# Kernel tuning notes

Measured on AMD Instinct MI355X. Metric: run time of the kernel, lower is better.

## Reference

```python
import jax, jax.numpy as jnp
import numpy as np

N_NODES = 50000
N_EDGES = 500000
IN_CH = 256
HID = 64
HEADS = 8
OUT_CH = 16
NEG_SLOPE = 0.2  # PyG GATConv default


def setup_inputs() -> dict:
    key = jax.random.key(0)
    ks = jax.random.split(key, 10)
    x = jax.random.normal(ks[0], (N_NODES, IN_CH), dtype=jnp.float32)
    edge_index = jax.random.randint(ks[1], (2, N_EDGES), 0, N_NODES, dtype=jnp.int64)
    s1 = 1.0 / np.sqrt(IN_CH)
    W1 = jax.random.uniform(ks[2], (IN_CH, HEADS * HID), jnp.float32, -s1, s1)
    att_src1 = jax.random.normal(ks[3], (HEADS, HID), dtype=jnp.float32) * 0.1
    att_dst1 = jax.random.normal(ks[4], (HEADS, HID), dtype=jnp.float32) * 0.1
    b1 = jnp.zeros((HEADS * HID,), jnp.float32)
    s2 = 1.0 / np.sqrt(HEADS * HID)
    W2 = jax.random.uniform(ks[5], (HEADS * HID, OUT_CH), jnp.float32, -s2, s2)
    att_src2 = jax.random.normal(ks[6], (1, OUT_CH), dtype=jnp.float32) * 0.1
    att_dst2 = jax.random.normal(ks[7], (1, OUT_CH), dtype=jnp.float32) * 0.1
    b2 = jnp.zeros((OUT_CH,), jnp.float32)
    return {"x": x, "edge_index": edge_index, "W1": W1, "att_src1": att_src1,
            "att_dst1": att_dst1, "b1": b1, "W2": W2, "att_src2": att_src2,
            "att_dst2": att_dst2, "b2": b2}


def _gat_conv(x, src, dst, W, att_src, att_dst, bias, heads, out_ch, concat, n_nodes):
    # Linear transform: [N, H, C]
    h = (x @ W).reshape(n_nodes, heads, out_ch)
    # Per-node attention logits: [N, H]
    a_src = jnp.einsum('nhc,hc->nh', h, att_src)
    a_dst = jnp.einsum('nhc,hc->nh', h, att_dst)
    # Edge-wise attention score (message src -> dst): [E, H]
    e = jax.nn.leaky_relu(a_src[src] + a_dst[dst], NEG_SLOPE)
    # Segment softmax over incoming edges of each destination node
    emax = jax.ops.segment_max(e, dst, num_segments=n_nodes)  # [N, H]
    emax = jnp.where(jnp.isfinite(emax), emax, 0.0)
    e = jnp.exp(e - emax[dst])
    denom = jax.ops.segment_sum(e, dst, num_segments=n_nodes)  # [N, H]
    alpha = e / (denom[dst] + 1e-16)
    # Weighted scatter-add aggregation: [N, H, C]
    msg = h[src] * alpha[:, :, None]
    out = jax.ops.segment_sum(msg, dst, num_segments=n_nodes)
    if concat:
        out = out.reshape(n_nodes, heads * out_ch)
    else:
        out = out.mean(axis=1)
    return out + bias


def reference(x, edge_index, W1, att_src1, att_dst1, b1, W2, att_src2, att_dst2, b2):
    n = x.shape[0]
    # PyG GATConv adds self-loops by default
    loops = jnp.arange(n, dtype=edge_index.dtype)
    src = jnp.concatenate([edge_index[0], loops])
    dst = jnp.concatenate([edge_index[1], loops])
    # dropout (p=0.6) is identity in eval mode
    h = _gat_conv(x, src, dst, W1, att_src1, att_dst1, b1, HEADS, HID, True, n)
    h = jax.nn.elu(h)
    out = _gat_conv(h, src, dst, W2, att_src2, att_dst2, b2, 1, OUT_CH, False, n)
    return jax.nn.log_softmax(out, axis=1)
```

## Files before the change

### kernel.cpp

```cpp
#include <hip/hip_runtime.h>
#include <math.h>

#define N_NODES 50000
#define N_EDGES 500000
#define IN_CH 256
#define D1 512
#define HEADS 8
#define HID 64
#define OUT_CH 16
#define NEG_SLOPE 0.2f

#define G1_BX 391
#define G1_BLOCKS (G1_BX * 4)
#define SCAT_BLOCKS ((N_EDGES + 255) / 256)

typedef __bf16 bf16x8 __attribute__((ext_vector_type(8)));
typedef float f32x4 __attribute__((ext_vector_type(4)));
typedef float f32x2 __attribute__((ext_vector_type(2)));

__device__ inline void fp8x8_to_f32(uint2 u, float* f) {
    f32x2 p0 = __builtin_amdgcn_cvt_pk_f32_fp8(u.x, false);
    f32x2 p1 = __builtin_amdgcn_cvt_pk_f32_fp8(u.x, true);
    f32x2 p2 = __builtin_amdgcn_cvt_pk_f32_fp8(u.y, false);
    f32x2 p3 = __builtin_amdgcn_cvt_pk_f32_fp8(u.y, true);
    f[0] = p0.x; f[1] = p0.y; f[2] = p1.x; f[3] = p1.y;
    f[4] = p2.x; f[5] = p2.y; f[6] = p3.x; f[7] = p3.y;
}

__device__ inline void fp8x16_to_f32(uint4 u, float* f) {
    fp8x8_to_f32(make_uint2(u.x, u.y), f);
    fp8x8_to_f32(make_uint2(u.z, u.w), f + 8);
}

__device__ inline unsigned char f32_to_fp8(float v) {
    return (unsigned char)(__builtin_amdgcn_cvt_pk_fp8_f32(v, v, 0, false) & 0xff);
}

__device__ inline float leaky_exp(float e) {
    float v = e > 0.f ? e : NEG_SLOPE * e;
    return __expf(v);
}

__device__ inline void gl_lds16(const __bf16* g, __bf16* l) {
    __builtin_amdgcn_global_load_lds(
        (const __attribute__((address_space(1))) unsigned int*)g,
        (__attribute__((address_space(3))) unsigned int*)l,
        16, 0, 0);
}

__global__ __launch_bounds__(256) void k_prep(const float* __restrict__ X,
                                              const float* __restrict__ W1,
                                              const float* __restrict__ W2,
                                              const int* __restrict__ edst,
                                              __bf16* __restrict__ Xb,
                                              __bf16* __restrict__ Wt,
                                              __bf16* __restrict__ Wt2,
                                              int* __restrict__ deg) {
    int t = blockIdx.x * 256 + threadIdx.x;
    int nthr = gridDim.x * 256;
    for (int i = t; i < N_NODES * IN_CH / 8; i += nthr) {
        size_t base = (size_t)i * 8;
        float4 v0 = *(const float4*)&X[base];
        float4 v1 = *(const float4*)&X[base + 4];
        __bf16 o[8] = {(__bf16)v0.x, (__bf16)v0.y, (__bf16)v0.z, (__bf16)v0.w,
                       (__bf16)v1.x, (__bf16)v1.y, (__bf16)v1.z, (__bf16)v1.w};
        *(uint4*)&Xb[base] = *(uint4*)o;
    }
    for (int i = t; i < D1 * IN_CH; i += nthr) {
        int n = i >> 8, k = i & 255;
        Wt[i] = (__bf16)W1[k * D1 + n];
    }
    for (int i = t; i < D1 * OUT_CH; i += nthr) {
        int n = i >> 9, k = i & 511;
        Wt2[i] = (__bf16)W2[k * OUT_CH + n];
    }
    for (int i = t; i < N_EDGES; i += nthr) atomicAdd(&deg[edst[i]], 1);
}

__global__ __launch_bounds__(256) void k_gemm1s(const __bf16* __restrict__ Xb,
                                                const __bf16* __restrict__ Wt,
                                                const float* __restrict__ att_src,
                                                const float* __restrict__ att_dst,
                                                unsigned char* __restrict__ Hf8,
                                                float* __restrict__ a_src1,
                                                float* __restrict__ a_dst1,
                                                const int* __restrict__ esrc,
                                                const int* __restrict__ edst,
                                                int* __restrict__ cursor,
                                                int* __restrict__ csr) {
    __shared__ __align__(16) __bf16 As[128 * 64];
    __shared__ __align__(16) __bf16 Bs[128 * 64];
    if (blockIdx.x >= G1_BLOCKS) {
        int e = (blockIdx.x - G1_BLOCKS) * 256 + threadIdx.x;
        if (e < N_EDGES) {
            int s = esrc[e], d = edst[e];
            int pos = atomicAdd(&cursor[d], 1);
            csr[pos] = s;
        }
        return;
    }
    int tid = threadIdx.x;
    int wid = tid >> 6, lane = tid & 63;
    int wr = wid >> 1, wc = wid & 1;
    int row0 = (blockIdx.x % G1_BX) * 128;
    int col0 = (blockIdx.x / G1_BX) * 128;
    int lq = lane >> 4;
    int lm = lane & 15;
    int sw = lm & 7;
    int r_st[4], g_st[4];
    #pragma unroll
    for (int it = 0; it < 4; ++it) {
        int idx = tid + it * 256;
        int r = idx >> 3;
        int p = idx & 7;
        r_st[it] = r;
        g_st[it] = (p ^ (r & 7)) * 8;
    }
    f32x4 acc[4][4] = {};
    for (int kt = 0; kt < IN_CH / 64; ++kt) {
        int k0 = kt * 64;
        #pragma unroll
        for (int it = 0; it < 4; ++it) {
            int idx = tid + it * 256;
            gl_lds16(&Xb[(size_t)(row0 + r_st[it]) * IN_CH + k0 + g_st[it]], &As[idx * 8]);
            gl_lds16(&Wt[(size_t)(col0 + r_st[it]) * IN_CH + k0 + g_st[it]], &Bs[idx * 8]);
        }
        __syncthreads();
        #pragma unroll
        for (int kt2 = 0; kt2 < 2; ++kt2) {
            bf16x8 af[4], bfr[4];
            #pragma unroll
            for (int i = 0; i < 4; ++i)
                af[i]  = *(bf16x8*)&As[(wr * 64 + i * 16 + lm) * 64 + (((kt2 * 4 + lq) ^ sw) * 8)];
            #pragma unroll
            for (int j = 0; j < 4; ++j)
                bfr[j] = *(bf16x8*)&Bs[(wc * 64 + j * 16 + lm) * 64 + (((kt2 * 4 + lq) ^ sw) * 8)];
            #pragma unroll
            for (int i = 0; i < 4; ++i)
                #pragma unroll
                for (int j = 0; j < 4; ++j)
                    acc[i][j] = __builtin_amdgcn_mfma_f32_16x16x32_bf16(af[i], bfr[j], acc[i][j], 0, 0, 0);
        }
        __syncthreads();
    }
    int head = (blockIdx.x / G1_BX) * 2 + wc;
    float as_v[4], ad_v[4];
    #pragma unroll
    for (int j = 0; j < 4; ++j) {
        as_v[j] = att_src[head * HID + j * 16 + lm];
        ad_v[j] = att_dst[head * HID + j * 16 + lm];
    }
    #pragma unroll
    for (int i = 0; i < 4; ++i) {
        int rbase = row0 + wr * 64 + i * 16 + lq * 4;
        #pragma unroll
        for (int r = 0; r < 4; ++r) {
            int grow = rbase + r;
            float ps = 0.f, pd = 0.f;
            #pragma unroll
            for (int j = 0; j < 4; ++j) {
                float v = acc[i][j][r];
                ps += v * as_v[j];
                pd += v * ad_v[j];
                if (grow < N_NODES)
                    Hf8[(size_t)grow * D1 + col0 + wc * 64 + j * 16 + lm] = f32_to_fp8(v);
            }
            #pragma unroll
            for (int off = 1; off < 16; off <<= 1) {
                ps += __shfl_xor(ps, off);
                pd += __shfl_xor(pd, off);
            }
            if (lm == 0 && grow < N_NODES) {
                a_src1[grow * HEADS + head] = ps;
                a_dst1[grow * HEADS + head] = pd;
            }
        }
    }
}

__global__ __launch_bounds__(1024) void k_scan1(const int* __restrict__ deg,
                                                int* __restrict__ offsets,
                                                int* __restrict__ bsum) {
    __shared__ int wsum[16];
    int tid = threadIdx.x, lane = tid & 63, wid = tid >> 6;
    int i = blockIdx.x * 1024 + tid;
    int v = (i < N_NODES) ? deg[i] : 0;
    int x = v;
    #pragma unroll
    for (int off = 1; off < 64; off <<= 1) {
        int t = __shfl_up(x, off);
        if (lane >= off) x += t;
    }
    if (lane == 63) wsum[wid] = x;
    __syncthreads();
    if (wid == 0) {
        int s = (lane < 16) ? wsum[lane] : 0;
        #pragma unroll
        for (int off = 1; off < 16; off <<= 1) {
            int t = __shfl_up(s, off);
            if (lane >= off) s += t;
        }
        if (lane < 16) wsum[lane] = s;
    }
    __syncthreads();
    int wbase = wid ? wsum[wid - 1] : 0;
    if (i < N_NODES) offsets[i] = wbase + x - v;
    if (tid == 1023) bsum[blockIdx.x] = wsum[15];
}

__global__ __launch_bounds__(256) void k_scan3(int* __restrict__ offsets,
                                               const int* __restrict__ bsum,
                                               int* __restrict__ cursor) {
    __shared__ int bpre_s[64];
    int tid = threadIdx.x;
    const int nb = (N_NODES + 1023) / 1024;
    if (tid < 64) {
        int v = (tid < nb) ? bsum[tid] : 0;
        int x = v;
        #pragma unroll
        for (int off = 1; off < 64; off <<= 1) {
            int t = __shfl_up(x, off);
            if (tid >= off) x += t;
        }
        bpre_s[tid] = x - v;
        if (blockIdx.x == 0 && tid == nb - 1) offsets[N_NODES] = x;
    }
    __syncthreads();
    int i = blockIdx.x * 256 + tid;
    if (i < N_NODES) {
        int o = offsets[i] + bpre_s[i >> 10];
        offsets[i] = o;
        cursor[i] = o;
    }
}

__device__ inline void agg1_pair(const unsigned char* __restrict__ Hf8,
                                 const float* __restrict__ a_src,
                                 int sA, int sB, int chb, int head, float ad_h,
                                 float* o, float& lsum) {
    uint4 uA = *(const uint4*)&Hf8[(size_t)sA * D1 + chb];
    uint4 uB = *(const uint4*)&Hf8[(size_t)sB * D1 + chb];
    float wA = leaky_exp(a_src[sA * HEADS + head] + ad_h);
    float wB = leaky_exp(a_src[sB * HEADS + head] + ad_h);
    float fA[16], fB[16];
    fp8x16_to_f32(uA, fA);
    fp8x16_to_f32(uB, fB);
    lsum += wA + wB;
    #pragma unroll
    for (int j = 0; j < 16; ++j) o[j] += wA * fA[j] + wB * fB[j];
}

__global__ __launch_bounds__(256) void k_agg1(const unsigned char* __restrict__ Hf8,
                                              const float* __restrict__ a_src,
                                              const float* __restrict__ a_dst,
                                              const int* __restrict__ offsets,
                                              const int* __restrict__ csr,
                                              const float* __restrict__ b1,
                                              __bf16* __restrict__ OUT) {
    int wave = (blockIdx.x * blockDim.x + threadIdx.x) >> 6;
    int lane = threadIdx.x & 63;
    if (wave >= N_NODES) return;
    int d = wave;
    int half = lane >> 5;
    int l32 = lane & 31;
    int chb = l32 * 16;
    int head = l32 >> 2;
    float ad_h = a_dst[d * HEADS + head];
    float o[16];
    #pragma unroll
    for (int j = 0; j < 16; ++j) o[j] = 0.f;
    float lsum = 0.f;
    if (half == 0) {
        float wself = leaky_exp(a_src[d * HEADS + head] + ad_h);
        uint4 hu = *(const uint4*)&Hf8[(size_t)d * D1 + chb];
        float hv[16];
        fp8x16_to_f32(hu, hv);
        lsum = wself;
        #pragma unroll
        for (int j = 0; j < 16; ++j) o[j] = wself * hv[j];
    }
    int beg = offsets[d], end = offsets[d + 1];
    int idx = beg;
    if (idx + 4 <= end) {
        int sA = csr[idx + half];
        int sB = csr[idx + 2 + half];
        for (; idx + 8 <= end; idx += 4) {
            int sA2 = csr[idx + 4 + half];
            int sB2 = csr[idx + 6 + half];
            agg1_pair(Hf8, a_src, sA, sB, chb, head, ad_h, o, lsum);
            sA = sA2; sB = sB2;
        }
        agg1_pair(Hf8, a_src, sA, sB, chb, head, ad_h, o, lsum);
        idx += 4;
    }
    for (; idx < end; idx += 2) {
        int e = idx + half;
        bool valid = e < end;
        int s = valid ? csr[e] : csr[idx];
        uint4 u = *(const uint4*)&Hf8[(size_t)s * D1 + chb];
        float w = valid ? leaky_exp(a_src[s * HEADS + head] + ad_h) : 0.f;
        float f[16];
        fp8x16_to_f32(u, f);
        lsum += w;
        #pragma unroll
        for (int j = 0; j < 16; ++j) o[j] += w * f[j];
    }
    #pragma unroll
    for (int j = 0; j < 16; ++j) o[j] += __shfl_xor(o[j], 32);
    lsum += __shfl_xor(lsum, 32);
    if (half == 0) {
        float inv = 1.0f / (lsum + 1e-16f);
        __bf16 r[16];
        #pragma unroll
        for (int j = 0; j < 16; ++j) {
            float v = o[j] * inv + b1[chb + j];
            v = v > 0.f ? v : (__expf(v) - 1.0f);
            r[j] = (__bf16)v;
        }
        *(uint4*)&OUT[(size_t)d * D1 + chb]     = *(uint4*)&r[0];
        *(uint4*)&OUT[(size_t)d * D1 + chb + 8] = *(uint4*)&r[8];
    }
}

__global__ __launch_bounds__(256) void k_gemm2_mfma(const __bf16* __restrict__ A,
                                                    const __bf16* __restrict__ Wt2,
                                                    const float* __restrict__ as2v,
                                                    const float* __restrict__ ad2v,
                                                    __bf16* __restrict__ H2,
                                                    float* __restrict__ a_src2,
                                                    float* __restrict__ a_dst2) {
    int tid = threadIdx.x;
    int wid = tid >> 6, lane = tid & 63;
    int lq = lane >> 4, lm = lane & 15;
    int row0 = blockIdx.x * 64 + wid * 16;
    int arow = row0 + lm;
    const __bf16* ap = A + (size_t)(arow < N_NODES ? arow : 0) * D1;
    f32x4 acc = {};
    #pragma unroll
    for (int k0 = 0; k0 < 16; ++k0) {
        bf16x8 af  = *(const bf16x8*)&ap[k0 * 32 + lq * 8];
        bf16x8 bfr = *(const bf16x8*)&Wt2[lm * D1 + k0 * 32 + lq * 8];
        acc = __builtin_amdgcn_mfma_f32_16x16x32_bf16(af, bfr, acc, 0, 0, 0);
    }
    float as_c = as2v[lm], ad_c = ad2v[lm];
    #pragma unroll
    for (int r = 0; r < 4; ++r) {
        int gr = row0 + lq * 4 + r;
        float v = acc[r];
        if (gr < N_NODES) H2[gr * OUT_CH + lm] = (__bf16)v;
        float ps = v * as_c, pd = v * ad_c;
        #pragma unroll
        for (int off = 1; off < 16; off <<= 1) {
            ps += __shfl_xor(ps, off);
            pd += __shfl_xor(pd, off);
        }
        if (lm == 0 && gr < N_NODES) { a_src2[gr] = ps; a_dst2[gr] = pd; }
    }
}

__device__ inline void agg2_pair(const __bf16* __restrict__ H2,
                                 const float* __restrict__ a_src,
                                 int s0, int s1, int c, float ad,
                                 float& o, float& lsum) {
    float h0 = (float)H2[s0 * OUT_CH + c];
    float h1 = (float)H2[s1 * OUT_CH + c];
    float wt0 = leaky_exp(a_src[s0] + ad);
    float wt1 = leaky_exp(a_src[s1] + ad);
    lsum += wt0 + wt1;
    o += wt0 * h0 + wt1 * h1;
}

__global__ __launch_bounds__(256) void k_agg2(const __bf16* __restrict__ H2,
                                              const float* __restrict__ a_src,
                                              const float* __restrict__ a_dst,
                                              const int* __restrict__ offsets,
                                              const int* __restrict__ csr,
                                              const float* __restrict__ b2,
                                              float* __restrict__ OUT) {
    int wave = (blockIdx.x * blockDim.x + threadIdx.x) >> 6;
    int lane = threadIdx.x & 63;
    if (wave >= N_NODES) return;
    int d = wave;
    int g = lane >> 4, c = lane & 15;
    float ad = a_dst[d];
    float o = 0.f, lsum = 0.f;
    if (g == 0) {
        float wself = leaky_exp(a_src[d] + ad);
        o = wself * (float)H2[d * OUT_CH + c];
        lsum = wself;
    }
    int beg = offsets[d], end = offsets[d + 1];
    int i0 = beg + g;
    if (i0 + 4 < end) {
        int s0 = csr[i0], s1 = csr[i0 + 4];
        for (; i0 + 12 < end; i0 += 8) {
            int t0 = csr[i0 + 8], t1 = csr[i0 + 12];
            agg2_pair(H2, a_src, s0, s1, c, ad, o, lsum);
            s0 = t0; s1 = t1;
        }
        agg2_pair(H2, a_src, s0, s1, c, ad, o, lsum);
        i0 += 8;
    }
    for (; i0 < end; i0 += 4) {
        int s = csr[i0];
        float wt = leaky_exp(a_src[s] + ad);
        float h = (float)H2[s * OUT_CH + c];
        lsum += wt;
        o += wt * h;
    }
    o += __shfl_xor(o, 16);  o += __shfl_xor(o, 32);
    lsum += __shfl_xor(lsum, 16);  lsum += __shfl_xor(lsum, 32);
    float v = o / (lsum + 1e-16f) + b2[c];
    float mx = v;
    #pragma unroll
    for (int off = 1; off < 16; off <<= 1) mx = fmaxf(mx, __shfl_xor(mx, off));
    float se = __expf(v - mx);
    #pragma unroll
    for (int off = 1; off < 16; off <<= 1) se += __shfl_xor(se, off);
    float res = v - mx - logf(se);
    if (lane < 16) OUT[d * OUT_CH + lane] = res;
}

extern "C" void kernel_launch(void* const* d_in, const int* in_sizes, int n_in,
                              void* d_out, int out_size, void* d_ws, size_t ws_size,
                              hipStream_t stream) {
    const float* x        = (const float*)d_in[0];
    const int*   ei       = (const int*)d_in[1];
    const float* W1       = (const float*)d_in[2];
    const float* att_src1 = (const float*)d_in[3];
    const float* att_dst1 = (const float*)d_in[4];
    const float* b1       = (const float*)d_in[5];
    const float* W2       = (const float*)d_in[6];
    const float* att_src2 = (const float*)d_in[7];
    const float* att_dst2 = (const float*)d_in[8];
    const float* b2       = (const float*)d_in[9];
    float* out = (float*)d_out;

    const int* esrc = ei;
    const int* edst = ei + N_EDGES;

    char* ws = (char*)d_ws;
    size_t off = 0;
    auto alloc = [&](size_t bytes) { char* p = ws + off; off = (off + bytes + 255) & ~(size_t)255; return p; };
    unsigned char* Hf8 = (unsigned char*)alloc((size_t)N_NODES * D1);
    __bf16* out1   = (__bf16*)alloc((size_t)N_NODES * D1 * 2);
    __bf16* Xb     = (__bf16*)alloc((size_t)N_NODES * IN_CH * 2);
    __bf16* Wt     = (__bf16*)alloc((size_t)D1 * IN_CH * 2);
    __bf16* Wt2    = (__bf16*)alloc((size_t)D1 * OUT_CH * 2);
    float* a_src1  = (float*)alloc((size_t)N_NODES * HEADS * 4);
    float* a_dst1  = (float*)alloc((size_t)N_NODES * HEADS * 4);
    __bf16* h2     = (__bf16*)alloc((size_t)N_NODES * OUT_CH * 2);
    float* a_src2  = (float*)alloc((size_t)N_NODES * 4);
    float* a_dst2  = (float*)alloc((size_t)N_NODES * 4);
    int*   deg     = (int*)alloc((size_t)N_NODES * 4);
    int*   offsets = (int*)alloc((size_t)(N_NODES + 1) * 4);
    int*   cursor  = (int*)alloc((size_t)N_NODES * 4);
    int*   csr     = (int*)alloc((size_t)N_EDGES * 4);
    int*   bsum    = (int*)alloc(64 * 4);
    (void)ws_size;

    hipMemsetAsync(deg, 0, (size_t)N_NODES * 4, stream);
    k_prep<<<512, 256, 0, stream>>>(x, W1, W2, edst, Xb, Wt, Wt2, deg);
    int nb = (N_NODES + 1023) / 1024;
    k_scan1<<<nb, 1024, 0, stream>>>(deg, offsets, bsum);
    k_scan3<<<(N_NODES + 255) / 256, 256, 0, stream>>>(offsets, bsum, cursor);
    k_gemm1s<<<G1_BLOCKS + SCAT_BLOCKS, 256, 0, stream>>>(
        Xb, Wt, att_src1, att_dst1, Hf8, a_src1, a_dst1, esrc, edst, cursor, csr);
    k_agg1<<<(N_NODES * 64 + 255) / 256, 256, 0, stream>>>(Hf8, a_src1, a_dst1, offsets, csr, b1, out1);
    k_gemm2_mfma<<<(N_NODES + 63) / 64, 256, 0, stream>>>(out1, Wt2, att_src2, att_dst2, h2, a_src2, a_dst2);
    k_agg2<<<(N_NODES * 64 + 255) / 256, 256, 0, stream>>>(h2, a_src2, a_dst2, offsets, csr, b2, out);
}
```

Baseline: 288.3 us.

## Replace LDS-tiled GEMM1 with register-direct MFMA and split edge scatter

The first-layer GEMM no longer stages tiles in LDS through global_load_lds. Each wave now loads A and B fragments straight from global memory and computes a 16x256 output strip, with 16 accumulators per wave. The CSR edge scatter moves out of the fused GEMM launch into its own kernel that runs after the scan, and the GEMM now launches before the scan. This drops LDS use and barriers, but it gives up shared-tile reuse, so B (weights) is re-read from global or L2 by every wave and register pressure goes up.

```diff
diff --git a/kernel.cpp b/kernel.cpp
--- a/kernel.cpp
+++ b/kernel.cpp
@@ -10,10 +10,6 @@
 #define OUT_CH 16
 #define NEG_SLOPE 0.2f
 
-#define G1_BX 391
-#define G1_BLOCKS (G1_BX * 4)
-#define SCAT_BLOCKS ((N_EDGES + 255) / 256)
-
 typedef __bf16 bf16x8 __attribute__((ext_vector_type(8)));
 typedef float f32x4 __attribute__((ext_vector_type(4)));
 typedef float f32x2 __attribute__((ext_vector_type(2)));
@@ -39,13 +35,6 @@
 __device__ inline float leaky_exp(float e) {
     float v = e > 0.f ? e : NEG_SLOPE * e;
     return __expf(v);
-}
-
-__device__ inline void gl_lds16(const __bf16* g, __bf16* l) {
-    __builtin_amdgcn_global_load_lds(
-        (const __attribute__((address_space(1))) unsigned int*)g,
-        (__attribute__((address_space(3))) unsigned int*)l,
-        16, 0, 0);
 }
 
 __global__ __launch_bounds__(256) void k_prep(const float* __restrict__ X,
@@ -77,102 +66,64 @@
     for (int i = t; i < N_EDGES; i += nthr) atomicAdd(&deg[edst[i]], 1);
 }
 
-__global__ __launch_bounds__(256) void k_gemm1s(const __bf16* __restrict__ Xb,
+__global__ __launch_bounds__(256) void k_gemm1b(const __bf16* __restrict__ Xb,
                                                 const __bf16* __restrict__ Wt,
                                                 const float* __restrict__ att_src,
                                                 const float* __restrict__ att_dst,
                                                 unsigned char* __restrict__ Hf8,
                                                 float* __restrict__ a_src1,
-                                                float* __restrict__ a_dst1,
-                                                const int* __restrict__ esrc,
-                                                const int* __restrict__ edst,
-                                                int* __restrict__ cursor,
-                                                int* __restrict__ csr) {
-    __shared__ __align__(16) __bf16 As[128 * 64];
-    __shared__ __align__(16) __bf16 Bs[128 * 64];
-    if (blockIdx.x >= G1_BLOCKS) {
-        int e = (blockIdx.x - G1_BLOCKS) * 256 + threadIdx.x;
-        if (e < N_EDGES) {
-            int s = esrc[e], d = edst[e];
-            int pos = atomicAdd(&cursor[d], 1);
-            csr[pos] = s;
-        }
-        return;
-    }
+                                                float* __restrict__ a_dst1) {
     int tid = threadIdx.x;
     int wid = tid >> 6, lane = tid & 63;
-    int wr = wid >> 1, wc = wid & 1;
-    int row0 = (blockIdx.x % G1_BX) * 128;
-    int col0 = (blockIdx.x / G1_BX) * 128;
-    int lq = lane >> 4;
-    int lm = lane & 15;
-    int sw = lm & 7;
-    int r_st[4], g_st[4];
-    #pragma unroll
-    for (int it = 0; it < 4; ++it) {
-        int idx = tid + it * 256;
-        int r = idx >> 3;
-        int p = idx & 7;
-        r_st[it] = r;
-        g_st[it] = (p ^ (r & 7)) * 8;
-    }
-    f32x4 acc[4][4] = {};
-    for (int kt = 0; kt < IN_CH / 64; ++kt) {
-        int k0 = kt * 64;
-        #pragma unroll
-        for (int it = 0; it < 4; ++it) {
-            int idx = tid + it * 256;
-            gl_lds16(&Xb[(size_t)(row0 + r_st[it]) * IN_CH + k0 + g_st[it]], &As[idx * 8]);
-            gl_lds16(&Wt[(size_t)(col0 + r_st[it]) * IN_CH + k0 + g_st[it]], &Bs[idx * 8]);
-        }
-        __syncthreads();
-        #pragma unroll
-        for (int kt2 = 0; kt2 < 2; ++kt2) {
-            bf16x8 af[4], bfr[4];
-            #pragma unroll
-            for (int i = 0; i < 4; ++i)
-                af[i]  = *(bf16x8*)&As[(wr * 64 + i * 16 + lm) * 64 + (((kt2 * 4 + lq) ^ sw) * 8)];
-            #pragma unroll
-            for (int j = 0; j < 4; ++j)
-                bfr[j] = *(bf16x8*)&Bs[(wc * 64 + j * 16 + lm) * 64 + (((kt2 * 4 + lq) ^ sw) * 8)];
-            #pragma unroll
-            for (int i = 0; i < 4; ++i)
-                #pragma unroll
-                for (int j = 0; j < 4; ++j)
-                    acc[i][j] = __builtin_amdgcn_mfma_f32_16x16x32_bf16(af[i], bfr[j], acc[i][j], 0, 0, 0);
-        }
-        __syncthreads();
-    }
-    int head = (blockIdx.x / G1_BX) * 2 + wc;
-    float as_v[4], ad_v[4];
-    #pragma unroll
-    for (int j = 0; j < 4; ++j) {
-        as_v[j] = att_src[head * HID + j * 16 + lm];
-        ad_v[j] = att_dst[head * HID + j * 16 + lm];
-    }
-    #pragma unroll
-    for (int i = 0; i < 4; ++i) {
-        int rbase = row0 + wr * 64 + i * 16 + lq * 4;
-        #pragma unroll
-        for (int r = 0; r < 4; ++r) {
-            int grow = rbase + r;
+    int lq = lane >> 4, lm = lane & 15;
+    int half = blockIdx.x & 1;
+    int rowt = blockIdx.x >> 1;
+    int row0 = rowt * 64 + wid * 16;
+    int c0 = half * 256;
+    int arow = row0 + lm;
+    if (arow >= N_NODES) arow = N_NODES - 1;
+    const __bf16* ap = Xb + (size_t)arow * IN_CH;
+    const __bf16* bp = Wt + (size_t)(c0 + lm) * IN_CH;
+    f32x4 acc[16] = {};
+    for (int k0 = 0; k0 < 8; ++k0) {
+        bf16x8 af = *(const bf16x8*)&ap[k0 * 32 + lq * 8];
+        #pragma unroll
+        for (int c = 0; c < 16; ++c) {
+            bf16x8 bfr = *(const bf16x8*)&bp[(size_t)c * 16 * IN_CH + k0 * 32 + lq * 8];
+            acc[c] = __builtin_amdgcn_mfma_f32_16x16x32_bf16(af, bfr, acc[c], 0, 0, 0);
+        }
+    }
+    float as_v[16], ad_v[16];
+    #pragma unroll
+    for (int c = 0; c < 16; ++c) {
+        int h = half * 4 + (c >> 2);
+        as_v[c] = att_src[h * HID + (c & 3) * 16 + lm];
+        ad_v[c] = att_dst[h * HID + (c & 3) * 16 + lm];
+    }
+    #pragma unroll
+    for (int r = 0; r < 4; ++r) {
+        int gr = row0 + lq * 4 + r;
+        bool ok = gr < N_NODES;
+        #pragma unroll
+        for (int h = 0; h < 4; ++h) {
             float ps = 0.f, pd = 0.f;
             #pragma unroll
-            for (int j = 0; j < 4; ++j) {
-                float v = acc[i][j][r];
-                ps += v * as_v[j];
-                pd += v * ad_v[j];
-                if (grow < N_NODES)
-                    Hf8[(size_t)grow * D1 + col0 + wc * 64 + j * 16 + lm] = f32_to_fp8(v);
+            for (int cc = 0; cc < 4; ++cc) {
+                int c = h * 4 + cc;
+                float v = acc[c][r];
+                ps += v * as_v[c];
+                pd += v * ad_v[c];
+                if (ok)
+                    Hf8[(size_t)gr * D1 + c0 + c * 16 + lm] = f32_to_fp8(v);
             }
             #pragma unroll
             for (int off = 1; off < 16; off <<= 1) {
                 ps += __shfl_xor(ps, off);
                 pd += __shfl_xor(pd, off);
             }
-            if (lm == 0 && grow < N_NODES) {
-                a_src1[grow * HEADS + head] = ps;
-                a_dst1[grow * HEADS + head] = pd;
+            if (lm == 0 && ok) {
+                a_src1[gr * HEADS + half * 4 + h] = ps;
+                a_dst1[gr * HEADS + half * 4 + h] = pd;
             }
         }
     }
@@ -232,6 +183,15 @@
         offsets[i] = o;
         cursor[i] = o;
     }
+}
+
+__global__ void k_scatter(const int* __restrict__ esrc, const int* __restrict__ edst,
+                          int* __restrict__ cursor, int* __restrict__ csr) {
+    int e = blockIdx.x * blockDim.x + threadIdx.x;
+    if (e >= N_EDGES) return;
+    int s = esrc[e], d = edst[e];
+    int pos = atomicAdd(&cursor[d], 1);
+    csr[pos] = s;
 }
 
 __device__ inline void agg1_pair(const unsigned char* __restrict__ Hf8,
@@ -461,11 +421,12 @@
 
     hipMemsetAsync(deg, 0, (size_t)N_NODES * 4, stream);
     k_prep<<<512, 256, 0, stream>>>(x, W1, W2, edst, Xb, Wt, Wt2, deg);
+    int g1_blocks = ((N_NODES + 63) / 64) * 2;
+    k_gemm1b<<<g1_blocks, 256, 0, stream>>>(Xb, Wt, att_src1, att_dst1, Hf8, a_src1, a_dst1);
     int nb = (N_NODES + 1023) / 1024;
     k_scan1<<<nb, 1024, 0, stream>>>(deg, offsets, bsum);
     k_scan3<<<(N_NODES + 255) / 256, 256, 0, stream>>>(offsets, bsum, cursor);
-    k_gemm1s<<<G1_BLOCKS + SCAT_BLOCKS, 256, 0, stream>>>(
-        Xb, Wt, att_src1, att_dst1, Hf8, a_src1, a_dst1, esrc, edst, cursor, csr);
+    k_scatter<<<(N_EDGES + 255) / 256, 256, 0, stream>>>(esrc, edst, cursor, csr);
     k_agg1<<<(N_NODES * 64 + 255) / 256, 256, 0, stream>>>(Hf8, a_src1, a_dst1, offsets, csr, b1, out1);
     k_gemm2_mfma<<<(N_NODES + 63) / 64, 256, 0, stream>>>(out1, Wt2, att_src2, att_dst2, h2, a_src2, a_dst2);
     k_agg2<<<(N_NODES * 64 + 255) / 256, 256, 0, stream>>>(h2, a_src2, a_dst2, offsets, csr, b2, out);
```

New measurement: 363.2 us. +26.0%, slower.
